# Performance work log

Hardware: AMD Instinct MI355X
Metric: run time of the kernel (lower is better)

The kernel has to match this reference:

```python
import jax, jax.numpy as jnp
import numpy as np

DIM = 16      # latent_dim == sec
SEC = 16
SUB = 16      # sub_sec
E = SEC * SUB # num_elements = 256
TH = 0.2
BATCH = 128
SL = BATCH // 2
TAU = 0.0001

bexpm = jax.vmap(jax.scipy.linalg.expm)


def _commut(ge):
    # commutative(div=dim): loop over K=E//DIM block pairs with cumulative block
    # swaps; loss = sum_k cumsum(per-pair sq-diff)[k] / (DIM*E)^2
    K = E // DIM
    basis = ge.reshape(DIM, DIM * E)                 # [d, d*E]
    bm = jnp.matmul(ge, basis).reshape(DIM * E, DIM * E)
    R = bm[:K * DIM, :K * DIM].reshape(K, DIM, K, DIM)
    c = 2.0 * ((R - jnp.transpose(R, (2, 1, 0, 3))) ** 2).sum((1, 3))  # [K,K]
    iu, ju = np.triu_indices(K, k=1)                 # lexicographic pair order
    return jnp.cumsum(c[iu, ju]).sum() / float((DIM * E) ** 2)


def _independent(z, ge, sec_idx):
    B = z.shape[0]
    syms = bexpm(ge)                                 # [E,d,d]
    diff = z - jnp.matmul(z, syms)                   # [E,B,d]
    d2 = (diff ** 2).reshape(-1, DIM)
    sparse = jnp.mean((d2.sum(-1) - d2.max(-1)) ** 2)
    par = diff.reshape(SEC, SUB * B, DIM)            # [SEC,M,d]
    nrm = jnp.linalg.norm(par, axis=-1, keepdims=True)
    nn_ = jnp.einsum('smi,sni->smn', nrm, nrm)       # [SEC,M,M]
    dd = jnp.einsum('smd,snd->smn', par, par)
    parallel = jnp.mean(-jnp.log((dd / nn_) ** 2 + 1e-9))
    sel = diff.reshape(SEC, SUB, B, DIM)[jnp.arange(SEC), sec_idx]
    sel = sel.reshape(SEC * B, DIM)
    sn = jnp.linalg.norm(sel, axis=-1, keepdims=True)
    ratio = (sel @ sel.T) / (sn @ sn.T)
    mask = jnp.asarray(1.0 - np.kron(np.eye(SEC, dtype=np.float32),
                                     np.ones((B, B), np.float32)))
    orth = jnp.mean((ratio ** 2) * mask)
    return orth, parallel, _commut(ge), sparse


def reference(mean, logvar, latent_z, group_elements, lin_w, lin_b,
              gumbel_noise, sec_idx):
    B = latent_z.shape[0]
    sl = B // 2
    mean1, mean2 = mean[:sl], mean[sl:]
    std1 = jnp.exp(0.5 * logvar[:sl])
    std2 = jnp.exp(0.5 * mean[sl:])   # (faithful to source bug: uses mean)
    z1, z2 = latent_z[:sl], latent_z[sl:]
    orth, parallel, commut, sparse = _independent(latent_z, group_elements, sec_idx)

    zd = z1 - z2
    target = (jnp.abs(zd) > TH).astype(jnp.int32).reshape(-1)   # [sl*SEC]
    feat = jnp.concatenate([mean1, std1, mean2, std2], -1)       # [sl,4d]
    prob = feat @ lin_w.T + lin_b                                # [sl,18*SEC]
    sector_logits = prob[:, :2 * SEC].reshape(-1, 2)             # [sl*SEC,2]
    p = jax.nn.softmax(sector_logits, -1)
    ls = jax.nn.log_softmax(p, -1)    # cross_entropy applied to softmax output
    sector_loss = -jnp.take_along_axis(ls, target[:, None], 1).sum() / sl

    attn = jax.nn.softmax((sector_logits + gumbel_noise) / TAU, -1)
    switch = jnp.where((attn[:, 0] >= 0.5) | (attn[:, 1] > 0.5), attn[:, 1], 0.0)
    switch = switch.reshape(sl, SEC)
    fprob = jax.nn.softmax(prob[:, 2 * SEC:].reshape(sl, SEC, SUB), -1)
    fprob = fprob.reshape(sl, E)
    w = jnp.repeat(switch, SUB, axis=-1) * fprob                 # [sl,E]
    syms = w[:, :, None, None] * group_elements[None]            # [sl,E,d,d]
    sub_syms = syms.reshape(sl, SEC, SUB, DIM, DIM).sum(2)       # [sl,SEC,d,d]
    S = syms.sum(1)                                              # [sl,d,d]
    fwd_syms = bexpm(S)
    inv_syms = bexpm(-S)
    attn_score = jnp.concatenate([switch, fprob], -1)            # [sl,SEC+E]

    tz1 = jnp.einsum('bd,bde->be', z1, fwd_syms)
    tz2 = jnp.einsum('bd,bde->be', z2, inv_syms)
    equivariant = jnp.mean((tz2 - z1) ** 2) + jnp.mean((tz1 - z2) ** 2)
    return (tz1, tz2, fwd_syms, equivariant, attn_score,
            orth, parallel, commut, sparse, sector_loss, sub_syms)


def setup_inputs() -> dict:
    key = jax.random.key(0)
    ks = jax.random.split(key, 7)
    mean = jax.random.normal(ks[0], (BATCH, DIM), jnp.float32)
    logvar = jax.random.normal(ks[1], (BATCH, DIM), jnp.float32)
    latent_z = jax.random.normal(ks[2], (BATCH, DIM), jnp.float32)
    group_elements = 0.1 * jax.random.normal(ks[3], (E, DIM, DIM), jnp.float32)
    lin_w = 0.1 * jax.random.normal(ks[4], ((SUB + 2) * SEC, 4 * DIM), jnp.float32)
    lin_b = jnp.zeros(((SUB + 2) * SEC,), jnp.float32)
    u = jax.random.uniform(ks[5], (SL * SEC, 2), jnp.float32, 1e-6, 1.0 - 1e-6)
    gumbel_noise = -jnp.log(-jnp.log(u))
    sec_idx = jax.random.randint(ks[6], (SEC,), 0, SEC, jnp.int32)
    return {'mean': mean, 'logvar': logvar, 'latent_z': latent_z,
            'group_elements': group_elements, 'lin_w': lin_w, 'lin_b': lin_b,
            'gumbel_noise': gumbel_noise, 'sec_idx': sec_idx}
```

## Files before the change

kernel.cpp:

```cpp
#include <hip/hip_runtime.h>
#include <math.h>

#define O_TZ1      0
#define O_TZ2      1024
#define O_FWD      2048
#define O_EQUI     18432
#define O_ATTN     18433
#define O_ORTH     35841
#define O_PAR      35842
#define O_COMM     35843
#define O_SPARSE   35844
#define O_SECLOSS  35845
#define O_SUB      35846

#define P_SECLOSS  0
#define P_SPARSE   64
#define P_CPAIR    320
#define P_EQUI     440
#define P_PAR      504
#define P_ORTH     2680

typedef short s16x8 __attribute__((ext_vector_type(8)));
typedef float f32x4 __attribute__((ext_vector_type(4)));

__device__ __forceinline__ void block_store(float v, float* red, int t, float* slot, float scale)
{
    red[t] = v;
    __syncthreads();
    for (int off = 128; off > 0; off >>= 1) { if (t < off) red[t] += red[t+off]; __syncthreads(); }
    if (t == 0) *slot = red[0] * scale;
}

__device__ __forceinline__ void block_store2(float v, float* red4, int t, float* slot, float scale)
{
    #pragma unroll
    for (int off = 32; off > 0; off >>= 1) v += __shfl_down(v, off);
    if ((t & 63) == 0) red4[t >> 6] = v;
    __syncthreads();
    if (t == 0) *slot = (red4[0] + red4[1] + red4[2] + red4[3]) * scale;
}

__device__ __forceinline__ unsigned short f2bf(float x)
{
    unsigned int u = __float_as_uint(x);
    u = (u + 0x7FFFu + ((u >> 16) & 1u)) >> 16;
    return (unsigned short)u;
}

__device__ __forceinline__ void expm_core(const float* __restrict__ src, float sign,
                                          float* sm, int* shi, int t)
{
    float* As = sm; float* T = sm + 256; float* P = sm + 512; float* rowsum = sm + 768;
    float a = src[t];
    As[t] = a;
    __syncthreads();
    if (t < 16) {
        float rs = 0.f;
        #pragma unroll
        for (int k = 0; k < 16; ++k) rs += fabsf(As[t*16+k]);
        rowsum[t] = rs;
    }
    __syncthreads();
    if (t == 0) {
        float nrm = 0.f;
        for (int i = 0; i < 16; ++i) nrm = fmaxf(nrm, rowsum[i]);
        int s = 0;
        if (nrm > 0.66f) { s = (int)ceilf(log2f(nrm * 1.51515f)); if (s < 0) s = 0; }
        *shi = s;
    }
    __syncthreads();
    int sq = *shi;
    float scale = sign * exp2f((float)(-sq));
    int i = t >> 4, j = t & 15;
    float as = a * scale;
    As[t] = as;
    T[t]  = ((i==j) ? 1.0f : 0.0f) + as;
    P[t]  = as;
    __syncthreads();
    for (int k = 2; k <= 8; ++k) {
        float accv = 0.f;
        #pragma unroll
        for (int m = 0; m < 16; ++m) accv += P[i*16+m]*As[m*16+j];
        float rk = 1.0f/(float)k;
        __syncthreads();
        float term = accv * rk;
        P[t] = term;
        T[t] += term;
        __syncthreads();
    }
    for (int q = 0; q < sq; ++q) {
        float accv = 0.f;
        #pragma unroll
        for (int m = 0; m < 16; ++m) accv += T[i*16+m]*T[m*16+j];
        __syncthreads();
        T[t] = accv;
        __syncthreads();
    }
}

template <bool DO_LOG>
__device__ __forceinline__ float gram_tile_lds(const unsigned short* __restrict__ diffb,
                                               short* tiles, int baseM, int baseN, int t)
{
    const uint4* gd = (const uint4*)diffb;
    #pragma unroll
    for (int q = 0; q < 2; ++q) {
        int idx = t + 256*q;
        int row = idx >> 1, half = idx & 1;
        int grow = (row < 128) ? (baseM + row) : (baseN + (row - 128));
        uint4 v = gd[grow*2 + half];
        *(uint4*)(tiles + row*24 + half*8) = v;
    }
    __syncthreads();
    int lane = t & 63, wave = t >> 6, quad = lane >> 4, col = lane & 15;
    s16x8 zf = {0,0,0,0,0,0,0,0};
    s16x8 A0=zf, A1=zf, B0=zf, B1=zf, B2=zf, B3=zf, B4=zf, B5=zf, B6=zf, B7=zf;
    if (quad < 2) {
        const short* tm_ = tiles;
        const short* tn_ = tiles + 128*24;
        A0 = *(const s16x8*)(tm_ + (wave*32      + col)*24 + quad*8);
        A1 = *(const s16x8*)(tm_ + (wave*32 + 16 + col)*24 + quad*8);
        B0 = *(const s16x8*)(tn_ + (  0 + col)*24 + quad*8);
        B1 = *(const s16x8*)(tn_ + ( 16 + col)*24 + quad*8);
        B2 = *(const s16x8*)(tn_ + ( 32 + col)*24 + quad*8);
        B3 = *(const s16x8*)(tn_ + ( 48 + col)*24 + quad*8);
        B4 = *(const s16x8*)(tn_ + ( 64 + col)*24 + quad*8);
        B5 = *(const s16x8*)(tn_ + ( 80 + col)*24 + quad*8);
        B6 = *(const s16x8*)(tn_ + ( 96 + col)*24 + quad*8);
        B7 = *(const s16x8*)(tn_ + (112 + col)*24 + quad*8);
    }
    f32x4 cz = {0.f, 0.f, 0.f, 0.f};
    float accf = 0.f;
#define GTILE(AF, BF) { \
    f32x4 c = __builtin_amdgcn_mfma_f32_16x16x32_bf16(AF, BF, cz, 0, 0, 0); \
    if (DO_LOG) { \
        float p0 = (c[0]*c[0] + 1e-9f) * (c[1]*c[1] + 1e-9f); \
        float p1 = (c[2]*c[2] + 1e-9f) * (c[3]*c[3] + 1e-9f); \
        accf += __log2f(p0 * p1); \
    } else { \
        accf += c[0]*c[0] + c[1]*c[1] + c[2]*c[2] + c[3]*c[3]; \
    } }
    GTILE(A0,B0) GTILE(A0,B1) GTILE(A0,B2) GTILE(A0,B3)
    GTILE(A0,B4) GTILE(A0,B5) GTILE(A0,B6) GTILE(A0,B7)
    GTILE(A1,B0) GTILE(A1,B1) GTILE(A1,B2) GTILE(A1,B3)
    GTILE(A1,B4) GTILE(A1,B5) GTILE(A1,B6) GTILE(A1,B7)
#undef GTILE
    return accf;
}

__global__ void k_stage1(const float* __restrict__ mean, const float* __restrict__ logvar,
                         const float* __restrict__ latent, const float* __restrict__ ge,
                         const float* __restrict__ lin_w, const float* __restrict__ lin_b,
                         const float* __restrict__ gumbel,
                         float* __restrict__ out, float* __restrict__ S_ws,
                         unsigned short* __restrict__ diffb, float* __restrict__ part)
{
    __shared__ float smem[4864];
    __shared__ int shi;
    int bid = blockIdx.x;
    int t = threadIdx.x;

    if (bid < 64) {
        int b = bid;
        float* feat = smem;
        float* probb = smem + 64;
        float* red16 = smem + 352;
        float* wrow = smem + 368;
        if (t < 64) {
            int k = t; float v;
            if (k < 16)       v = mean[b*16 + k];
            else if (k < 32)  v = expf(0.5f * logvar[b*16 + (k-16)]);
            else if (k < 48)  v = mean[(64+b)*16 + (k-32)];
            else              v = expf(0.5f * mean[(64+b)*16 + (k-48)]);
            feat[k] = v;
        }
        __syncthreads();
        for (int j = t; j < 288; j += 256) {
            float a = lin_b[j];
            const float* wr = lin_w + j*64;
            #pragma unroll
            for (int k = 0; k < 64; ++k) a += feat[k]*wr[k];
            probb[j] = a;
        }
        __syncthreads();
        if (t < 16) {
            int s = t;
            float l0 = probb[2*s], l1 = probb[2*s+1];
            float M = fmaxf(l0,l1);
            float e0 = expf(l0-M), e1 = expf(l1-M);
            float Z = e0+e1;
            float p0 = e0/Z, p1 = e1/Z;
            float M2 = fmaxf(p0,p1);
            float lse = M2 + logf(expf(p0-M2)+expf(p1-M2));
            float ls0 = p0 - lse, ls1 = p1 - lse;
            float z1v = latent[b*16+s], z2v = latent[(64+b)*16+s];
            int tt = (fabsf(z1v - z2v) > 0.2f) ? 1 : 0;
            red16[s] = -(tt ? ls1 : ls0);
            int r = b*16 + s;
            float x0 = (l0 + gumbel[2*r])   * 10000.0f;
            float x1 = (l1 + gumbel[2*r+1]) * 10000.0f;
            float Ma = fmaxf(x0,x1);
            float a0 = expf(x0-Ma), a1 = expf(x1-Ma);
            float Za = a0+a1;
            a0 /= Za; a1 /= Za;
            float sw = ((a0 >= 0.5f) || (a1 > 0.5f)) ? a1 : 0.0f;
            out[O_ATTN + b*272 + s] = sw;
            const float* fl = &probb[32 + s*16];
            float mf = fl[0];
            #pragma unroll
            for (int u = 1; u < 16; ++u) mf = fmaxf(mf, fl[u]);
            float ex[16]; float Zf = 0.f;
            #pragma unroll
            for (int u = 0; u < 16; ++u) { ex[u] = expf(fl[u]-mf); Zf += ex[u]; }
            float rZ = 1.0f/Zf;
            #pragma unroll
            for (int u = 0; u < 16; ++u) {
                float fp = ex[u]*rZ;
                out[O_ATTN + b*272 + 16 + s*16 + u] = fp;
                wrow[s*16 + u] = sw*fp;
            }
        }
        __syncthreads();
        if (t == 0) {
            float s = 0.f;
            for (int i = 0; i < 16; ++i) s += red16[i];
            part[P_SECLOSS + b] = s;
        }
        float Stot = 0.f;
        for (int s = 0; s < 16; ++s) {
            float a = 0.f;
            #pragma unroll
            for (int u = 0; u < 16; ++u)
                a += wrow[s*16+u] * ge[(s*16+u)*256 + t];
            out[O_SUB + b*4096 + s*256 + t] = a;
            Stot += a;
        }
        S_ws[b*256 + t] = Stot;
    } else if (bid < 320) {
        int e = bid - 64;
        float* zsh = smem + 784;
        float* red = smem + 2832;
        #pragma unroll
        for (int q = 0; q < 8; ++q) zsh[t+256*q] = latent[t+256*q];
        expm_core(ge + e*256, 1.0f, smem, &shi, t);
        const float* T = smem + 256;
        float pv = 0.f;
        if (t < 128) {
            float zr[16];
            #pragma unroll
            for (int k = 0; k < 16; ++k) zr[k] = zsh[t*16+k];
            float dv[16];
            float sum = 0.f, mx = 0.f;
            #pragma unroll
            for (int d = 0; d < 16; ++d) {
                float a = 0.f;
                #pragma unroll
                for (int k = 0; k < 16; ++k) a += zr[k]*T[k*16+d];
                float v = zr[d] - a;
                dv[d] = v;
                float v2 = v*v;
                sum += v2; mx = fmaxf(mx, v2);
            }
            float sm2 = sum - mx;
            pv = sm2*sm2;
            float ri = 1.0f / sqrtf(sum);
            unsigned int pk[8];
            #pragma unroll
            for (int d = 0; d < 8; ++d) {
                unsigned short h0 = f2bf(dv[2*d]   * ri);
                unsigned short h1 = f2bf(dv[2*d+1] * ri);
                pk[d] = (unsigned int)h0 | ((unsigned int)h1 << 16);
            }
            uint4* dst = (uint4*)(diffb + (size_t)(e*128 + t)*16);
            dst[0] = make_uint4(pk[0], pk[1], pk[2], pk[3]);
            dst[1] = make_uint4(pk[4], pk[5], pk[6], pk[7]);
        }
        block_store(pv, red, t, part + P_SPARSE + e, 1.0f);
    } else {
        int idx = bid - 320;
        float* G = smem;
        float* gA = smem + 4096;
        float* gB = smem + 4352;
        float* red = smem + 4608;
        int a2 = 0, cnt = 15, rem = idx;
        while (rem >= cnt) { rem -= cnt; a2++; cnt--; }
        int b2 = a2 + 1 + rem;
        #pragma unroll
        for (int q = 0; q < 16; ++q) {
            int ii = t + 256*q;
            int k = ii >> 8, x = ii & 255;
            G[ii] = ge[k*16*256 + x];
        }
        gA[t] = ge[a2*256+t];
        gB[t] = ge[b2*256+t];
        __syncthreads();
        int i = t >> 4, j = t & 15;
        float v1 = 0.f, v2 = 0.f;
        #pragma unroll
        for (int k = 0; k < 16; ++k) {
            v1 += gA[i*16+k]*G[k*256 + b2*16 + j];
            v2 += gB[i*16+k]*G[k*256 + a2*16 + j];
        }
        float d = v1 - v2;
        block_store(d*d, red, t, part + P_CPAIR + idx, 2.0f);
    }
}

__global__ void __launch_bounds__(256) k_stage2(const float* __restrict__ latent,
                                                const float* __restrict__ S_ws,
                                                const unsigned short* __restrict__ diffb,
                                                const int* __restrict__ sec_idx,
                                                float* __restrict__ out,
                                                float* __restrict__ part)
{
    __shared__ float smem[3328];
    __shared__ int shi;
    int bid = blockIdx.x;
    int t = threadIdx.x;
    float* red4 = smem + 3072;

    if (bid < 64) {
        int b = bid;
        expm_core(S_ws + b*256, 1.0f, smem, &shi, t);
        const float* T = smem + 256;
        out[O_FWD + b*256 + t] = T[t];
        float t1 = 0.f, z1d = 0.f, z2d = 0.f;
        if (t < 16) {
            int d = t;
            #pragma unroll
            for (int k = 0; k < 16; ++k) t1 += latent[b*16+k] * T[k*16+d];
            out[O_TZ1 + b*16 + d] = t1;
            z1d = latent[b*16+d];
            z2d = latent[(64+b)*16+d];
        }
        expm_core(S_ws + b*256, -1.0f, smem, &shi, t);
        float t2 = 0.f, ep = 0.f;
        if (t < 16) {
            int d = t;
            #pragma unroll
            for (int k = 0; k < 16; ++k) t2 += latent[(64+b)*16+k] * T[k*16+d];
            out[O_TZ2 + b*16 + d] = t2;
            ep = (t2 - z1d)*(t2 - z1d) + (t1 - z2d)*(t1 - z2d);
        }
        block_store2(ep, red4, t, part + P_EQUI + b, 1.0f);
    } else if (bid < 2240) {
        int tile = bid - 64;
        int s = tile & 15;
        int r = tile >> 4;
        int tm = 0;
        while (r >= 16 - tm) { r -= 16 - tm; tm++; }
        int tn = tm + r;
        float accf = gram_tile_lds<true>(diffb, (short*)smem, s*2048 + tm*128, s*2048 + tn*128, t);
        float wt = (tm == tn) ? 1.0f : 2.0f;
        block_store2(accf, red4, t, part + P_PAR + tile, wt);
    } else {
        int idx = bid - 2240;
        int sm = 0, cnt = 15, rem = idx;
        while (rem >= cnt) { rem -= cnt; sm++; cnt--; }
        int sn = sm + 1 + rem;
        int em = sm*16 + sec_idx[sm];
        int en = sn*16 + sec_idx[sn];
        float accf = gram_tile_lds<false>(diffb, (short*)smem, em*128, en*128, t);
        block_store2(accf, red4, t, part + P_ORTH + idx, 2.0f);
    }
}

__global__ void k_final(const float* __restrict__ part, float* __restrict__ out)
{
    __shared__ double dred[256];
    int t = threadIdx.x;

    double local = 0.0;
    for (int i = t; i < 2176; i += 256) local += (double)part[P_PAR + i];
    dred[t] = local;
    __syncthreads();
    for (int off = 128; off > 0; off >>= 1) { if (t < off) dred[t] += dred[t+off]; __syncthreads(); }
    double s_par = dred[0];
    __syncthreads();

    local = 0.0;
    if (t < 120) local += (double)part[P_ORTH + t];
    dred[t] = local;
    __syncthreads();
    for (int off = 128; off > 0; off >>= 1) { if (t < off) dred[t] += dred[t+off]; __syncthreads(); }
    double s_orth = dred[0];
    __syncthreads();

    local = 0.0;
    if (t < 64) local += (double)part[P_EQUI + t];
    dred[t] = local;
    __syncthreads();
    for (int off = 128; off > 0; off >>= 1) { if (t < off) dred[t] += dred[t+off]; __syncthreads(); }
    double s_equi = dred[0];
    __syncthreads();

    local = (t < 64) ? (double)part[P_SECLOSS + t] : 0.0;
    dred[t] = local;
    __syncthreads();
    for (int off = 128; off > 0; off >>= 1) { if (t < off) dred[t] += dred[t+off]; __syncthreads(); }
    double s_sec = dred[0];
    __syncthreads();

    dred[t] = (double)part[P_SPARSE + t];
    __syncthreads();
    for (int off = 128; off > 0; off >>= 1) { if (t < off) dred[t] += dred[t+off]; __syncthreads(); }
    double s_spa = dred[0];
    __syncthreads();

    local = 0.0;
    if (t < 120) local = (double)(120 - t) * (double)part[P_CPAIR + t];
    dred[t] = local;
    __syncthreads();
    for (int off = 128; off > 0; off >>= 1) { if (t < off) dred[t] += dred[t+off]; __syncthreads(); }

    if (t == 0) {
        out[O_COMM]    = (float)(dred[0] / 16777216.0);
        out[O_EQUI]    = (float)(s_equi / 1024.0);
        out[O_ORTH]    = (float)(s_orth / (2048.0*2048.0));
        out[O_PAR]     = (float)(-s_par * 0.6931471805599453 / 67108864.0);
        out[O_SPARSE]  = (float)(s_spa / 32768.0);
        out[O_SECLOSS] = (float)(s_sec / 64.0);
    }
}

extern "C" void kernel_launch(void* const* d_in, const int* in_sizes, int n_in,
                              void* d_out, int out_size, void* d_ws, size_t ws_size,
                              hipStream_t stream)
{
    const float* mean    = (const float*)d_in[0];
    const float* logvar  = (const float*)d_in[1];
    const float* latent  = (const float*)d_in[2];
    const float* ge      = (const float*)d_in[3];
    const float* lin_w   = (const float*)d_in[4];
    const float* lin_b   = (const float*)d_in[5];
    const float* gumbel  = (const float*)d_in[6];
    const int*   sec_idx = (const int*)d_in[7];
    float* out = (float*)d_out;

    char* ws = (char*)d_ws;
    float* part = (float*)ws;
    float* S_ws = (float*)(ws + 16384);
    unsigned short* diffb = (unsigned short*)(ws + 81920);

    k_stage1<<<440,  256, 0, stream>>>(mean, logvar, latent, ge, lin_w, lin_b, gumbel,
                                       out, S_ws, diffb, part);
    k_stage2<<<2360, 256, 0, stream>>>(latent, S_ws, diffb, sec_idx, out, part);
    k_final <<<1,    256, 0, stream>>>(part, out);
}
```

Before: 93.29 us.

## Fuse final reduction into stage2, split fwd/inv expm across blocks, speed up expm

Removes the separate single-block final kernel: each stage2 block bumps an atomic counter, and the last block to finish does the double-precision reductions. The forward and inverse matrix exponentials, previously run one after the other in a single block, now go to separate blocks, so stage2 grows by 64 blocks. The expm core is rewritten to use shuffle-based row sums, a padded transposed copy for vectorised float4 dot products, and double-buffered ping-pong LDS with half the barriers. Tree reductions are replaced by wave-shuffle reductions. The risk is the threadfence/atomic ordering and resetting the counter in stage1.

```diff
diff --git a/kernel.cpp b/kernel.cpp
--- a/kernel.cpp
+++ b/kernel.cpp
@@ -17,19 +17,12 @@
 #define P_SPARSE   64
 #define P_CPAIR    320
 #define P_EQUI     440
-#define P_PAR      504
-#define P_ORTH     2680
+#define P_PAR      568
+#define P_ORTH     2744
+#define P_CNT      2864
 
 typedef short s16x8 __attribute__((ext_vector_type(8)));
 typedef float f32x4 __attribute__((ext_vector_type(4)));
-
-__device__ __forceinline__ void block_store(float v, float* red, int t, float* slot, float scale)
-{
-    red[t] = v;
-    __syncthreads();
-    for (int off = 128; off > 0; off >>= 1) { if (t < off) red[t] += red[t+off]; __syncthreads(); }
-    if (t == 0) *slot = red[0] * scale;
-}
 
 __device__ __forceinline__ void block_store2(float v, float* red4, int t, float* slot, float scale)
 {
@@ -47,55 +40,85 @@
     return (unsigned short)u;
 }
 
-__device__ __forceinline__ void expm_core(const float* __restrict__ src, float sign,
-                                          float* sm, int* shi, int t)
-{
-    float* As = sm; float* T = sm + 256; float* P = sm + 512; float* rowsum = sm + 768;
+__device__ __forceinline__ float dot16(const float* arow, const float* brow)
+{
+    const f32x4* pa = (const f32x4*)arow;
+    const f32x4* pb = (const f32x4*)brow;
+    f32x4 s = pa[0] * pb[0];
+    s += pa[1] * pb[1];
+    s += pa[2] * pb[2];
+    s += pa[3] * pb[3];
+    return (s[0] + s[1]) + (s[2] + s[3]);
+}
+
+__device__ __forceinline__ void expm_core2(const float* __restrict__ src, float sign,
+                                           float* sm, int* shi, int t,
+                                           const float** Tres, const float** TTres)
+{
+    float* As  = sm;
+    float* AsT = sm + 256;
+    float* P0  = sm + 576;
+    float* P1  = sm + 832;
+    float* T0  = sm + 1088;
+    float* TT0 = sm + 1344;
+    float* T1  = sm + 1664;
+    float* TT1 = sm + 1920;
+    float* rowsum = sm + 2240;
+    int i = t >> 4, j = t & 15;
+
     float a = src[t];
-    As[t] = a;
-    __syncthreads();
-    if (t < 16) {
-        float rs = 0.f;
-        #pragma unroll
-        for (int k = 0; k < 16; ++k) rs += fabsf(As[t*16+k]);
-        rowsum[t] = rs;
-    }
+    float av = fabsf(a);
+    av += __shfl_xor(av, 1);
+    av += __shfl_xor(av, 2);
+    av += __shfl_xor(av, 4);
+    av += __shfl_xor(av, 8);
+    if (j == 0) rowsum[i] = av;
     __syncthreads();
     if (t == 0) {
         float nrm = 0.f;
-        for (int i = 0; i < 16; ++i) nrm = fmaxf(nrm, rowsum[i]);
+        #pragma unroll
+        for (int r = 0; r < 16; ++r) nrm = fmaxf(nrm, rowsum[r]);
         int s = 0;
         if (nrm > 0.66f) { s = (int)ceilf(log2f(nrm * 1.51515f)); if (s < 0) s = 0; }
         *shi = s;
     }
     __syncthreads();
     int sq = *shi;
-    float scale = sign * exp2f((float)(-sq));
-    int i = t >> 4, j = t & 15;
-    float as = a * scale;
+    float as = a * sign * exp2f((float)(-sq));
     As[t] = as;
-    T[t]  = ((i==j) ? 1.0f : 0.0f) + as;
-    P[t]  = as;
-    __syncthreads();
+    AsT[j*20 + i] = as;
+    float tval = ((i == j) ? 1.0f : 0.0f) + as;
+    __syncthreads();
+
+    const float* Pc = As;
+    float* Pn = P0;
+    #pragma unroll
     for (int k = 2; k <= 8; ++k) {
-        float accv = 0.f;
-        #pragma unroll
-        for (int m = 0; m < 16; ++m) accv += P[i*16+m]*As[m*16+j];
-        float rk = 1.0f/(float)k;
-        __syncthreads();
-        float term = accv * rk;
-        P[t] = term;
-        T[t] += term;
-        __syncthreads();
-    }
+        float accv = dot16(Pc + i*16, AsT + j*20);
+        float term = accv * (1.0f / (float)k);
+        Pn[t] = term;
+        tval += term;
+        __syncthreads();
+        const float* tmp = Pn;
+        Pn = (Pn == P0) ? P1 : P0;
+        Pc = tmp;
+    }
+
+    float* Tc = T0; float* TTc = TT0; float* Tn = T1; float* TTn = TT1;
+    Tc[t] = tval;
+    TTc[j*20 + i] = tval;
+    __syncthreads();
     for (int q = 0; q < sq; ++q) {
-        float accv = 0.f;
-        #pragma unroll
-        for (int m = 0; m < 16; ++m) accv += T[i*16+m]*T[m*16+j];
-        __syncthreads();
-        T[t] = accv;
-        __syncthreads();
-    }
+        float accv = dot16(Tc + i*16, TTc + j*20);
+        Tn[t] = accv;
+        TTn[j*20 + i] = accv;
+        __syncthreads();
+        float* x;
+        x = Tc;  Tc  = Tn;  Tn  = x;
+        x = TTc; TTc = TTn; TTn = x;
+    }
+    *Tres = Tc;
+    *TTres = TTc;
 }
 
 template <bool DO_LOG>
@@ -155,12 +178,13 @@
                          float* __restrict__ out, float* __restrict__ S_ws,
                          unsigned short* __restrict__ diffb, float* __restrict__ part)
 {
-    __shared__ float smem[4864];
+    __shared__ float smem[4880];
     __shared__ int shi;
     int bid = blockIdx.x;
     int t = threadIdx.x;
 
     if (bid < 64) {
+        if (bid == 0 && t == 0) *(int*)(part + P_CNT) = 0;
         int b = bid;
         float* feat = smem;
         float* probb = smem + 64;
@@ -238,24 +262,30 @@
         S_ws[b*256 + t] = Stot;
     } else if (bid < 320) {
         int e = bid - 64;
-        float* zsh = smem + 784;
-        float* red = smem + 2832;
+        float* zsh  = smem + 2304;
+        float* red4 = smem + 4864;
         #pragma unroll
-        for (int q = 0; q < 8; ++q) zsh[t+256*q] = latent[t+256*q];
-        expm_core(ge + e*256, 1.0f, smem, &shi, t);
-        const float* T = smem + 256;
+        for (int q = 0; q < 8; ++q) {
+            int idx = t + 256*q;
+            zsh[(idx >> 4)*20 + (idx & 15)] = latent[idx];
+        }
+        const float *T, *TT;
+        expm_core2(ge + e*256, 1.0f, smem, &shi, t, &T, &TT);
         float pv = 0.f;
         if (t < 128) {
             float zr[16];
             #pragma unroll
-            for (int k = 0; k < 16; ++k) zr[k] = zsh[t*16+k];
+            for (int k = 0; k < 16; ++k) zr[k] = zsh[t*20 + k];
             float dv[16];
             float sum = 0.f, mx = 0.f;
             #pragma unroll
             for (int d = 0; d < 16; ++d) {
+                const f32x4* tr = (const f32x4*)(TT + d*20);
+                f32x4 q0 = tr[0], q1 = tr[1], q2 = tr[2], q3 = tr[3];
                 float a = 0.f;
                 #pragma unroll
-                for (int k = 0; k < 16; ++k) a += zr[k]*T[k*16+d];
+                for (int k = 0; k < 4; ++k)
+                    a += zr[k]*q0[k] + zr[4+k]*q1[k] + zr[8+k]*q2[k] + zr[12+k]*q3[k];
                 float v = zr[d] - a;
                 dv[d] = v;
                 float v2 = v*v;
@@ -275,13 +305,13 @@
             dst[0] = make_uint4(pk[0], pk[1], pk[2], pk[3]);
             dst[1] = make_uint4(pk[4], pk[5], pk[6], pk[7]);
         }
-        block_store(pv, red, t, part + P_SPARSE + e, 1.0f);
+        block_store2(pv, red4, t, part + P_SPARSE + e, 1.0f);
     } else {
         int idx = bid - 320;
-        float* G = smem;
-        float* gA = smem + 4096;
-        float* gB = smem + 4352;
-        float* red = smem + 4608;
+        float* G   = smem;
+        float* gA  = smem + 4096;
+        float* gB  = smem + 4352;
+        float* red4 = smem + 4608;
         int a2 = 0, cnt = 15, rem = idx;
         while (rem >= cnt) { rem -= cnt; a2++; cnt--; }
         int b2 = a2 + 1 + rem;
@@ -302,7 +332,7 @@
             v2 += gB[i*16+k]*G[k*256 + a2*16 + j];
         }
         float d = v1 - v2;
-        block_store(d*d, red, t, part + P_CPAIR + idx, 2.0f);
+        block_store2(d*d, red4, t, part + P_CPAIR + idx, 2.0f);
     }
 }
 
@@ -315,36 +345,40 @@
 {
     __shared__ float smem[3328];
     __shared__ int shi;
+    __shared__ int lastflag;
     int bid = blockIdx.x;
     int t = threadIdx.x;
     float* red4 = smem + 3072;
 
-    if (bid < 64) {
-        int b = bid;
-        expm_core(S_ws + b*256, 1.0f, smem, &shi, t);
-        const float* T = smem + 256;
-        out[O_FWD + b*256 + t] = T[t];
-        float t1 = 0.f, z1d = 0.f, z2d = 0.f;
+    if (bid < 128) {
+        int b = bid & 63;
+        float sign = (bid < 64) ? 1.0f : -1.0f;
+        const float *T, *TT;
+        expm_core2(S_ws + b*256, sign, smem, &shi, t, &T, &TT);
+        if (bid < 64) out[O_FWD + b*256 + t] = T[t];
+        float ep = 0.f;
         if (t < 16) {
             int d = t;
-            #pragma unroll
-            for (int k = 0; k < 16; ++k) t1 += latent[b*16+k] * T[k*16+d];
-            out[O_TZ1 + b*16 + d] = t1;
-            z1d = latent[b*16+d];
-            z2d = latent[(64+b)*16+d];
-        }
-        expm_core(S_ws + b*256, -1.0f, smem, &shi, t);
-        float t2 = 0.f, ep = 0.f;
-        if (t < 16) {
-            int d = t;
-            #pragma unroll
-            for (int k = 0; k < 16; ++k) t2 += latent[(64+b)*16+k] * T[k*16+d];
-            out[O_TZ2 + b*16 + d] = t2;
-            ep = (t2 - z1d)*(t2 - z1d) + (t1 - z2d)*(t1 - z2d);
-        }
-        block_store2(ep, red4, t, part + P_EQUI + b, 1.0f);
-    } else if (bid < 2240) {
-        int tile = bid - 64;
+            const float* zrow = latent + ((bid < 64) ? b*16 : (64+b)*16);
+            const f32x4* tr = (const f32x4*)(TT + d*20);
+            f32x4 q0 = tr[0], q1 = tr[1], q2 = tr[2], q3 = tr[3];
+            float acc = 0.f;
+            #pragma unroll
+            for (int k = 0; k < 4; ++k)
+                acc += zrow[k]*q0[k] + zrow[4+k]*q1[k] + zrow[8+k]*q2[k] + zrow[12+k]*q3[k];
+            if (bid < 64) {
+                out[O_TZ1 + b*16 + d] = acc;
+                float z2d = latent[(64+b)*16 + d];
+                ep = (acc - z2d)*(acc - z2d);
+            } else {
+                out[O_TZ2 + b*16 + d] = acc;
+                float z1d = latent[b*16 + d];
+                ep = (acc - z1d)*(acc - z1d);
+            }
+        }
+        block_store2(ep, red4, t, part + P_EQUI + bid, 1.0f);
+    } else if (bid < 2304) {
+        int tile = bid - 128;
         int s = tile & 15;
         int r = tile >> 4;
         int tm = 0;
@@ -354,7 +388,7 @@
         float wt = (tm == tn) ? 1.0f : 2.0f;
         block_store2(accf, red4, t, part + P_PAR + tile, wt);
     } else {
-        int idx = bid - 2240;
+        int idx = bid - 2304;
         int sm = 0, cnt = 15, rem = idx;
         while (rem >= cnt) { rem -= cnt; sm++; cnt--; }
         int sn = sm + 1 + rem;
@@ -363,63 +397,52 @@
         float accf = gram_tile_lds<false>(diffb, (short*)smem, em*128, en*128, t);
         block_store2(accf, red4, t, part + P_ORTH + idx, 2.0f);
     }
-}
-
-__global__ void k_final(const float* __restrict__ part, float* __restrict__ out)
-{
-    __shared__ double dred[256];
-    int t = threadIdx.x;
-
-    double local = 0.0;
-    for (int i = t; i < 2176; i += 256) local += (double)part[P_PAR + i];
-    dred[t] = local;
-    __syncthreads();
-    for (int off = 128; off > 0; off >>= 1) { if (t < off) dred[t] += dred[t+off]; __syncthreads(); }
-    double s_par = dred[0];
-    __syncthreads();
-
-    local = 0.0;
-    if (t < 120) local += (double)part[P_ORTH + t];
-    dred[t] = local;
-    __syncthreads();
-    for (int off = 128; off > 0; off >>= 1) { if (t < off) dred[t] += dred[t+off]; __syncthreads(); }
-    double s_orth = dred[0];
-    __syncthreads();
-
-    local = 0.0;
-    if (t < 64) local += (double)part[P_EQUI + t];
-    dred[t] = local;
-    __syncthreads();
-    for (int off = 128; off > 0; off >>= 1) { if (t < off) dred[t] += dred[t+off]; __syncthreads(); }
-    double s_equi = dred[0];
-    __syncthreads();
-
-    local = (t < 64) ? (double)part[P_SECLOSS + t] : 0.0;
-    dred[t] = local;
-    __syncthreads();
-    for (int off = 128; off > 0; off >>= 1) { if (t < off) dred[t] += dred[t+off]; __syncthreads(); }
-    double s_sec = dred[0];
-    __syncthreads();
-
-    dred[t] = (double)part[P_SPARSE + t];
-    __syncthreads();
-    for (int off = 128; off > 0; off >>= 1) { if (t < off) dred[t] += dred[t+off]; __syncthreads(); }
-    double s_spa = dred[0];
-    __syncthreads();
-
-    local = 0.0;
-    if (t < 120) local = (double)(120 - t) * (double)part[P_CPAIR + t];
-    dred[t] = local;
-    __syncthreads();
-    for (int off = 128; off > 0; off >>= 1) { if (t < off) dred[t] += dred[t+off]; __syncthreads(); }
-
+
+    __threadfence();
     if (t == 0) {
-        out[O_COMM]    = (float)(dred[0] / 16777216.0);
-        out[O_EQUI]    = (float)(s_equi / 1024.0);
-        out[O_ORTH]    = (float)(s_orth / (2048.0*2048.0));
-        out[O_PAR]     = (float)(-s_par * 0.6931471805599453 / 67108864.0);
-        out[O_SPARSE]  = (float)(s_spa / 32768.0);
-        out[O_SECLOSS] = (float)(s_sec / 64.0);
+        int old = atomicAdd((int*)(part + P_CNT), 1);
+        lastflag = (old == (int)gridDim.x - 1);
+    }
+    __syncthreads();
+    if (lastflag) {
+        __threadfence();
+        double par = 0.0, orth = 0.0, equi = 0.0, sec = 0.0, spa = 0.0, com = 0.0;
+        for (int i2 = t; i2 < 2176; i2 += 256) par += (double)part[P_PAR + i2];
+        if (t < 120) orth = (double)part[P_ORTH + t];
+        if (t < 128) equi = (double)part[P_EQUI + t];
+        if (t < 64)  sec  = (double)part[P_SECLOSS + t];
+        spa = (double)part[P_SPARSE + t];
+        if (t < 120) com = (double)(120 - t) * (double)part[P_CPAIR + t];
+        #pragma unroll
+        for (int off = 32; off > 0; off >>= 1) {
+            par  += __shfl_down(par,  off);
+            orth += __shfl_down(orth, off);
+            equi += __shfl_down(equi, off);
+            sec  += __shfl_down(sec,  off);
+            spa  += __shfl_down(spa,  off);
+            com  += __shfl_down(com,  off);
+        }
+        double* dsc = (double*)smem;
+        int w = t >> 6;
+        if ((t & 63) == 0) {
+            dsc[w*6+0] = par;  dsc[w*6+1] = orth; dsc[w*6+2] = equi;
+            dsc[w*6+3] = sec;  dsc[w*6+4] = spa;  dsc[w*6+5] = com;
+        }
+        __syncthreads();
+        if (t == 0) {
+            par  = dsc[0]  + dsc[6]  + dsc[12] + dsc[18];
+            orth = dsc[1]  + dsc[7]  + dsc[13] + dsc[19];
+            equi = dsc[2]  + dsc[8]  + dsc[14] + dsc[20];
+            sec  = dsc[3]  + dsc[9]  + dsc[15] + dsc[21];
+            spa  = dsc[4]  + dsc[10] + dsc[16] + dsc[22];
+            com  = dsc[5]  + dsc[11] + dsc[17] + dsc[23];
+            out[O_COMM]    = (float)(com / 16777216.0);
+            out[O_EQUI]    = (float)(equi / 1024.0);
+            out[O_ORTH]    = (float)(orth / (2048.0*2048.0));
+            out[O_PAR]     = (float)(-par * 0.6931471805599453 / 67108864.0);
+            out[O_SPARSE]  = (float)(spa / 32768.0);
+            out[O_SECLOSS] = (float)(sec / 64.0);
+        }
     }
 }
 
@@ -444,6 +467,5 @@
 
     k_stage1<<<440,  256, 0, stream>>>(mean, logvar, latent, ge, lin_w, lin_b, gumbel,
                                        out, S_ws, diffb, part);
-    k_stage2<<<2360, 256, 0, stream>>>(latent, S_ws, diffb, sec_idx, out, part);
-    k_final <<<1,    256, 0, stream>>>(part, out);
-}
+    k_stage2<<<2424, 256, 0, stream>>>(latent, S_ws, diffb, sec_idx, out, part);
+}
```

Measured after the change: 236.8 us. 2.54x slower.
